# Kernel tuning notes

Measured on AMD Instinct MI355X. Metric: run time of the kernel, lower is better.

The kernel has to match this reference:

```python
import jax, jax.numpy as jnp
import numpy as np

N_NODES = 50000
N_EDGES = 1200000
N_OD = 10000
D_NODE = 16
D_EDGE = 8
HID = 64
N_LAYERS = 3
K_MIN = 1.0
K_MAX = 50.0


def setup_inputs() -> dict:
    key = jax.random.key(0)
    ks = jax.random.split(key, 24)
    s = 0.05
    inp = {
        "node_features": jax.random.normal(ks[0], (N_NODES, D_NODE), jnp.float32),
        "edge_index": jax.random.randint(ks[1], (2, N_EDGES), 0, N_NODES, jnp.int32),
        "edge_features": jax.random.normal(ks[2], (N_EDGES, D_EDGE), jnp.float32),
        "od_pairs": jax.random.randint(ks[3], (2, N_OD), 0, N_NODES, jnp.int32),
        "traffic_stats": jax.random.normal(ks[4], (4,), jnp.float32),
        # projections
        "Wn": jax.random.normal(ks[5], (D_NODE, HID), jnp.float32) * s,
        "bn": jnp.zeros((HID,), jnp.float32),
        "We": jax.random.normal(ks[6], (D_EDGE, HID), jnp.float32) * s,
        "be": jnp.zeros((HID,), jnp.float32),
        # stacked GNN layer weights: message MLP on [h_src, e], update MLP on [h, agg]
        "Wm": jax.random.normal(ks[7], (N_LAYERS, 2 * HID, HID), jnp.float32) * s,
        "bm": jnp.zeros((N_LAYERS, HID), jnp.float32),
        "Wu": jax.random.normal(ks[8], (N_LAYERS, 2 * HID, HID), jnp.float32) * s,
        "bu": jnp.zeros((N_LAYERS, HID), jnp.float32),
        # per-flow score MLP on [h_src, h_dst]
        "Ws1": jax.random.normal(ks[9], (2 * HID, HID), jnp.float32) * s,
        "bs1": jnp.zeros((HID,), jnp.float32),
        "Ws2": jax.random.normal(ks[10], (HID, 1), jnp.float32) * s,
        "bs2": jnp.zeros((1,), jnp.float32),
        # DynamicKHead: Linear(HID+4,32) -> ReLU -> Linear(32,16) -> ReLU -> Linear(16,1)
        "Wk1": jax.random.normal(ks[11], (HID + 4, 32), jnp.float32) * s,
        "bk1": jnp.zeros((32,), jnp.float32),
        "Wk2": jax.random.normal(ks[12], (32, 16), jnp.float32) * s,
        "bk2": jnp.zeros((16,), jnp.float32),
        "Wk3": jax.random.normal(ks[13], (16, 1), jnp.float32) * s,
        "bk3": jnp.zeros((1,), jnp.float32),
    }
    return inp


def _forward(node_features, edge_features, traffic_stats,
             Wn, bn, We, be, Wm, bm, Wu, bu,
             Ws1, bs1, Ws2, bs2, Wk1, bk1, Wk2, bk2, Wk3, bk3,
             edge_index, od_pairs):
    relu = jax.nn.relu
    h = relu(node_features @ Wn + bn)          # [N, HID]
    e = relu(edge_features @ We + be)          # [E, HID]
    src, dst = edge_index[0], edge_index[1]
    for l in range(N_LAYERS):
        # gather-compute-scatter message passing with edge features
        m = relu(jnp.concatenate([h[src], e], axis=-1) @ Wm[l] + bm[l])  # [E, HID]
        agg = jax.ops.segment_sum(m, dst, num_segments=N_NODES)          # [N, HID]
        h = relu(jnp.concatenate([h, agg], axis=-1) @ Wu[l] + bu[l]) + h  # residual
    # per-flow scores from OD endpoint embeddings
    hp = jnp.concatenate([h[od_pairs[0]], h[od_pairs[1]]], axis=-1)      # [P, 2*HID]
    scores = (relu(hp @ Ws1 + bs1) @ Ws2 + bs2).squeeze(-1)              # [P]
    # dynamic-K head (dropout = identity in eval)
    graph_embed = h.mean(axis=0)                                          # [HID]
    x = jnp.concatenate([graph_embed, traffic_stats], axis=-1)
    raw = (relu(relu(x @ Wk1 + bk1) @ Wk2 + bk2) @ Wk3 + bk3).squeeze(-1)
    k_continuous = K_MIN + jax.nn.sigmoid(raw) * (K_MAX - K_MIN)
    return scores, k_continuous


def reference(node_features, edge_index, edge_features, od_pairs, traffic_stats,
              Wn, bn, We, be, Wm, bm, Wu, bu,
              Ws1, bs1, Ws2, bs2, Wk1, bk1, Wk2, bk2, Wk3, bk3):
    return _forward(node_features, edge_features, traffic_stats,
                    Wn, bn, We, be, Wm, bm, Wu, bu,
                    Ws1, bs1, Ws2, bs2, Wk1, bk1, Wk2, bk2, Wk3, bk3,
                    edge_index, od_pairs)
```

## Files before the change

### kernel.cpp

```cpp
#include <hip/hip_runtime.h>
#include <hip/hip_bf16.h>

#define OFF_WN   0
#define OFF_BN   1024
#define OFF_WE   1088
#define OFF_BE   1600
#define OFF_WM   1664
#define OFF_BM   26240
#define OFF_WU   26432
#define OFF_BU   51008
#define OFF_WS1  51200
#define OFF_BS1  59392
#define OFF_WS2  59456
#define OFF_BS2  59520
#define OFF_WK1  59521
#define OFF_BK1  61697
#define OFF_WK2  61729
#define OFF_BK2  62241
#define OFF_WK3  62257
#define OFF_BK3  62273
#define OFF_TS   62274
#define OFF_GSUM 62278
#define OFF_FLAG 62344
#define OFF_BSUM 62400
#define OFF_BOFF 62900
#define OFF_H    65536

typedef __attribute__((ext_vector_type(8))) short bfrag;
typedef __attribute__((ext_vector_type(4))) float ffrag;

__device__ __forceinline__ float bf2f(unsigned short u) {
    unsigned int i = ((unsigned int)u) << 16;
    float f;
    __builtin_memcpy(&f, &i, sizeof(f));
    return f;
}
__device__ __forceinline__ float bflo(unsigned int u) {
    unsigned int i = u << 16;
    float f; __builtin_memcpy(&f, &i, sizeof(f)); return f;
}
__device__ __forceinline__ float bfhi(unsigned int u) {
    unsigned int i = u & 0xffff0000u;
    float f; __builtin_memcpy(&f, &i, sizeof(f)); return f;
}
__device__ __forceinline__ unsigned int f2bf_rne(float f) {
    unsigned int u; __builtin_memcpy(&u, &f, 4);
    return (u + 0x7fffu + ((u >> 16) & 1u)) >> 16;
}
__device__ __forceinline__ unsigned int pack2bf(float a, float b) {
    return f2bf_rne(a) | (f2bf_rne(b) << 16);
}
__device__ __forceinline__ unsigned int cvt_pk_bf16(float a, float b) {
    unsigned int r;
    asm("v_cvt_pk_bf16_f32 %0, %1, %2" : "=v"(r) : "v"(a), "v"(b));
    return r;
}

__global__ void detect_dtype_kernel(const unsigned short* __restrict__ nf,
                                    int* __restrict__ flag) {
    int t = threadIdx.x;
    float m = 0.f;
    for (int i = t; i < 1024; i += 64) {
        float v = fabsf(bf2f(nf[i]));
        if (!isnan(v)) m = fmaxf(m, v);
        else m = 1e30f;
    }
    for (int o = 32; o > 0; o >>= 1) m = fmaxf(m, __shfl_down(m, o));
    if (t == 0) flag[0] = (m > 1e6f) ? 1 : 0;
}

struct ConvArgs {
    const void* src[19];
    int off[19];
    int n[19];
};

__global__ __launch_bounds__(256) void convert_all_kernel(
        ConvArgs a, float* __restrict__ ws, const int* __restrict__ flagp) {
    int isf32 = *flagp;
    int ai = blockIdx.y;
    int i  = blockIdx.x * blockDim.x + threadIdx.x;
    if (i < a.n[ai]) {
        float v = isf32 ? ((const float*)a.src[ai])[i]
                        : bf2f(((const unsigned short*)a.src[ai])[i]);
        ws[a.off[ai] + i] = v;
    }
}

__global__ __launch_bounds__(256) void wtrans_prep_kernel(
        const float* __restrict__ ws, short* __restrict__ Wb) {
    int idx = blockIdx.x * 256 + threadIdx.x;
    if (idx < 12288) {
        int l = idx >> 12, rem = idx & 4095, n = rem >> 6, k = rem & 63;
        Wb[idx] = (short)f2bf_rne(ws[OFF_WM + l * 8192 + 4096 + k * 64 + n]);
    } else if (idx < 24576) {
        int j = idx - 12288;
        int l = j >> 12, rem = j & 4095, n = rem >> 6, k = rem & 63;
        Wb[idx] = (short)f2bf_rne(ws[OFF_WM + l * 8192 + k * 64 + n]);
    } else if (idx < 49152) {
        int j = idx - 24576;
        int l = j >> 13, rem = j & 8191, n = rem >> 7, k = rem & 127;
        Wb[idx] = (short)f2bf_rne(ws[OFF_WU + l * 8192 + k * 64 + n]);
    } else if (idx < 51200) {
        int j = idx - 49152;
        int n = j >> 5, k = j & 31;
        Wb[idx] = (k < 8) ? (short)f2bf_rne(ws[OFF_WE + k * 64 + n]) : (short)0;
    } else if (idx < 59392) {
        int j = idx - 51200;
        int n = j >> 7, k = j & 127;
        Wb[idx] = (short)f2bf_rne(ws[OFF_WS1 + k * 64 + n]);
    }
}

__global__ __launch_bounds__(256) void node_proj_kernel(
        const void* __restrict__ nf, const float* __restrict__ ws,
        float* __restrict__ h, int N, const int* __restrict__ flagp) {
    int idx = blockIdx.x * blockDim.x + threadIdx.x;
    if (idx >= N * 64) return;
    int isf32 = *flagp;
    int i = idx >> 6, c = idx & 63;
    const float* Wn = ws + OFF_WN;
    float acc = ws[OFF_BN + c];
    float x[16];
    if (isf32) {
        const float* row = (const float*)nf + (size_t)i * 16;
#pragma unroll
        for (int k = 0; k < 16; ++k) x[k] = row[k];
    } else {
        const unsigned short* row = (const unsigned short*)nf + (size_t)i * 16;
#pragma unroll
        for (int k = 0; k < 16; ++k) x[k] = bf2f(row[k]);
    }
#pragma unroll
    for (int k = 0; k < 16; ++k) acc = fmaf(x[k], Wn[k * 64 + c], acc);
    h[idx] = fmaxf(acc, 0.f);
}

__global__ __launch_bounds__(256) void count_kernel(
        const int* __restrict__ dst, int* __restrict__ deg, int E) {
    int e = blockIdx.x * blockDim.x + threadIdx.x;
    if (e < E) atomicAdd(&deg[dst[e]], 1);
}

__global__ __launch_bounds__(256) void scan_blocks_kernel(
        const int* __restrict__ deg, int* __restrict__ incl,
        int* __restrict__ bsum, int N) {
    int tid = threadIdx.x;
    int gid = blockIdx.x * 256 + tid;
    int v = (gid < N) ? deg[gid] : 0;
    int lane = tid & 63, w = tid >> 6;
    int x = v;
#pragma unroll
    for (int o = 1; o < 64; o <<= 1) {
        int y = __shfl_up(x, o);
        if (lane >= o) x += y;
    }
    __shared__ int wsum[4];
    __shared__ int woff[4];
    if (lane == 63) wsum[w] = x;
    __syncthreads();
    if (tid == 0) {
        int a = 0;
#pragma unroll
        for (int i = 0; i < 4; ++i) { woff[i] = a; a += wsum[i]; }
    }
    __syncthreads();
    x += woff[w];
    if (gid < N) incl[gid] = x;
    if (tid == 255) bsum[blockIdx.x] = x;
}

__global__ __launch_bounds__(256) void scan_bsum_kernel(
        const int* __restrict__ bsum, int* __restrict__ boff, int nb) {
    __shared__ int sh[256];
    int tid = threadIdx.x;
    int carry = 0;
    for (int base = 0; base < nb; base += 256) {
        int v = (base + tid < nb) ? bsum[base + tid] : 0;
        sh[tid] = v;
        __syncthreads();
        for (int o = 1; o < 256; o <<= 1) {
            int t = (tid >= o) ? sh[tid - o] : 0;
            __syncthreads();
            sh[tid] += t;
            __syncthreads();
        }
        if (base + tid < nb) boff[base + tid] = carry + sh[tid] - v;
        __syncthreads();
        carry += sh[255];
        __syncthreads();
    }
}

__global__ __launch_bounds__(256) void scan_finalize_kernel(
        const int* __restrict__ deg, const int* __restrict__ incl,
        const int* __restrict__ boff, int* __restrict__ out,
        int* __restrict__ cursor, int N, int tailval) {
    int gid = blockIdx.x * 256 + threadIdx.x;
    if (gid < N) {
        int ex = boff[blockIdx.x] + incl[gid] - deg[gid];
        out[gid] = ex;
        cursor[gid] = ex;
    }
    if (gid == 0) out[N] = tailval;
}

__global__ __launch_bounds__(256) void fill_kernel(
        const int* __restrict__ src, const int* __restrict__ dst,
        const void* __restrict__ ef, int* __restrict__ cursor,
        int* __restrict__ eid, int* __restrict__ srcs,
        float* __restrict__ rec, int E, int big,
        const int* __restrict__ flagp) {
    int e = blockIdx.x * blockDim.x + threadIdx.x;
    if (e >= E) return;
    int d = dst[e];
    int pos = atomicAdd(&cursor[d], 1);
    if (big) {
        unsigned p01, p23, p45, p67;
        if (*flagp) {
            const float4* p = (const float4*)ef + (size_t)e * 2;
            float4 a = p[0], b = p[1];
            p01 = pack2bf(a.x, a.y); p23 = pack2bf(a.z, a.w);
            p45 = pack2bf(b.x, b.y); p67 = pack2bf(b.z, b.w);
        } else {
            uint4 r = ((const uint4*)ef)[e];
            p01 = r.x; p23 = r.y; p45 = r.z; p67 = r.w;
        }
        float* o = rec + (size_t)pos * 8;
        *(uint4*)o = make_uint4((unsigned)src[e], (unsigned)d, p01, p23);
        *(uint2*)(o + 4) = make_uint2(p45, p67);
    } else {
        eid[pos] = e;
        srcs[pos] = src[e];
    }
}

__global__ __launch_bounds__(256) void spans_kernel(
        const int* __restrict__ off, int* __restrict__ spans, int N) {
    int i = blockIdx.x * blockDim.x + threadIdx.x;
    if (i >= N) return;
    int k0 = off[i], k1 = off[i + 1];
    spans[i] = (k1 > k0) ? (((k1 - 1) >> 6) - (k0 >> 6) + 1) : 0;
}

__global__ __launch_bounds__(256) void nodeA_mfma_kernel(
        const short* __restrict__ W1T, const float* __restrict__ bm,
        const float* __restrict__ h, float* __restrict__ A, int N) {
    __shared__ short lds_w[64 * 72];
    __shared__ short lds_x[4][64 * 72];
    const int tid = threadIdx.x, wid = tid >> 6, lane = tid & 63;
    const int r = lane & 15, q = lane >> 4;
    const int nb0 = blockIdx.x * 256 + wid * 64;

#pragma unroll
    for (int j = 0; j < 2; ++j) {
        int f8 = (tid * 2 + j) * 8;
        int row = f8 >> 6, k = f8 & 63;
        *(uint4*)&lds_w[row * 72 + k] = ((const uint4*)W1T)[tid * 2 + j];
    }
    short* xt = &lds_x[wid][0];
#pragma unroll 1
    for (int it = 0; it < 16; ++it) {
        int f4 = it * 64 + lane;
        int node = f4 >> 4, c4 = f4 & 15;
        int gn = nb0 + node; if (gn >= N) gn = N - 1;
        float4 v = ((const float4*)h)[(size_t)gn * 16 + c4];
        *(uint2*)&xt[node * 72 + c4 * 4] =
            make_uint2(pack2bf(v.x, v.y), pack2bf(v.z, v.w));
    }
    __syncthreads();

    bfrag bg[4][2];
#pragma unroll
    for (int ni = 0; ni < 4; ++ni)
#pragma unroll
        for (int ki = 0; ki < 2; ++ki)
            bg[ni][ki] = *(const bfrag*)&lds_w[(ni * 16 + r) * 72 + ki * 32 + q * 8];
    float buv[4];
#pragma unroll
    for (int ni = 0; ni < 4; ++ni) buv[ni] = bm[ni * 16 + r];

    ffrag C[4][4];
#pragma unroll
    for (int mi = 0; mi < 4; ++mi) {
        bfrag af[2];
#pragma unroll
        for (int ki = 0; ki < 2; ++ki)
            af[ki] = *(const bfrag*)&xt[(mi * 16 + r) * 72 + ki * 32 + q * 8];
#pragma unroll
        for (int ni = 0; ni < 4; ++ni) {
            ffrag c = {buv[ni], buv[ni], buv[ni], buv[ni]};
            c = __builtin_amdgcn_mfma_f32_16x16x32_bf16(af[0], bg[ni][0], c, 0, 0, 0);
            c = __builtin_amdgcn_mfma_f32_16x16x32_bf16(af[1], bg[ni][1], c, 0, 0, 0);
            C[mi][ni] = c;
        }
    }
#pragma unroll
    for (int mi = 0; mi < 4; ++mi)
#pragma unroll
        for (int rr = 0; rr < 4; ++rr) {
            int gn = nb0 + mi * 16 + q * 4 + rr;
            if (gn < N) {
#pragma unroll
                for (int ni = 0; ni < 4; ++ni)
                    A[(size_t)gn * 64 + ni * 16 + r] = C[mi][ni][rr];
            }
        }
}

__global__ __launch_bounds__(256, 4) void msg_mfma_red(
        const short* __restrict__ WeT, const float* __restrict__ be,
        const short* __restrict__ WbT, const float* __restrict__ rec,
        const float* __restrict__ A, float* __restrict__ pbuf,
        const int* __restrict__ off, const int* __restrict__ pstart, int E) {
    __shared__ short lds_ev[4][64 * 72];
    __shared__ int   lds_src[4][64];
    const int tid = threadIdx.x;
    const int wid = tid >> 6, lane = tid & 63;
    const int w = blockIdx.x * 4 + wid;
    if (w * 64 >= E) return;
    const int slot = w * 64 + lane;
    const int slotc = (slot < E) ? slot : (E - 1);

    const float* rbase = rec + (size_t)slotc * 8;
    uint4 r0 = *(const uint4*)rbase;
    uint2 r1 = *(const uint2*)(rbase + 4);
    int s  = (int)r0.x;
    int di = (int)r0.y;
    int pstv = pstart[di];
    int offv = off[di];
    lds_src[wid][lane] = s;

    short* evb = &lds_ev[wid][0];
    short* evrow = evb + lane * 72;
    *(uint4*)(evrow) = make_uint4(r0.z, r0.w, r1.x, r1.y);
    uint4 z4 = make_uint4(0u, 0u, 0u, 0u);
    *(uint4*)(evrow + 8)  = z4;
    *(uint4*)(evrow + 16) = z4;
    *(uint4*)(evrow + 24) = z4;

    const int r = lane & 15, q = lane >> 4;

    bfrag afe[4];
#pragma unroll
    for (int mi = 0; mi < 4; ++mi)
        afe[mi] = *(const bfrag*)(evb + (mi * 16 + r) * 72 + q * 8);

#pragma unroll
    for (int ni = 0; ni < 4; ++ni) {
        bfrag bge = *(const bfrag*)(WeT + (ni * 16 + r) * 32 + q * 8);
        float4 b4 = *(const float4*)(be + ni * 16 + q * 4);
#pragma unroll
        for (int mi = 0; mi < 4; ++mi) {
            ffrag c = {b4.x, b4.y, b4.z, b4.w};
            c = __builtin_amdgcn_mfma_f32_16x16x32_bf16(bge, afe[mi], c, 0, 0, 0);
            unsigned lo = cvt_pk_bf16(fmaxf(c[0], 0.f), fmaxf(c[1], 0.f));
            unsigned hi = cvt_pk_bf16(fmaxf(c[2], 0.f), fmaxf(c[3], 0.f));
            *(uint2*)(evb + (mi * 16 + r) * 72 + ni * 16 + q * 4) =
                make_uint2(lo, hi);
        }
    }

    bfrag af[4][2];
#pragma unroll
    for (int mi = 0; mi < 4; ++mi)
#pragma unroll
        for (int ki = 0; ki < 2; ++ki)
            af[mi][ki] = *(const bfrag*)(evb + (mi * 16 + r) * 72 + ki * 32 + q * 8);

    const float* ap[4][4];
#pragma unroll
    for (int mi = 0; mi < 4; ++mi) {
        int4 sr = *(const int4*)&lds_src[wid][mi * 16 + q * 4];
        ap[mi][0] = A + (size_t)sr.x * 64 + r;
        ap[mi][1] = A + (size_t)sr.y * 64 + r;
        ap[mi][2] = A + (size_t)sr.z * 64 + r;
        ap[mi][3] = A + (size_t)sr.w * 64 + r;
    }

#pragma unroll
    for (int ni = 0; ni < 4; ++ni) {
        bfrag bg0 = *(const bfrag*)(WbT + (ni * 16 + r) * 64 + q * 8);
        bfrag bg1 = *(const bfrag*)(WbT + (ni * 16 + r) * 64 + 32 + q * 8);
        ffrag C[4];
#pragma unroll
        for (int mi = 0; mi < 4; ++mi) {
            C[mi][0] = ap[mi][0][ni * 16];
            C[mi][1] = ap[mi][1][ni * 16];
            C[mi][2] = ap[mi][2][ni * 16];
            C[mi][3] = ap[mi][3][ni * 16];
        }
#pragma unroll
        for (int mi = 0; mi < 4; ++mi) {
            C[mi] = __builtin_amdgcn_mfma_f32_16x16x32_bf16(af[mi][0], bg0, C[mi], 0, 0, 0);
            C[mi] = __builtin_amdgcn_mfma_f32_16x16x32_bf16(af[mi][1], bg1, C[mi], 0, 0, 0);
        }
#pragma unroll
        for (int mi = 0; mi < 4; ++mi) {
            unsigned lo = cvt_pk_bf16(fmaxf(C[mi][0], 0.f), fmaxf(C[mi][1], 0.f));
            unsigned hi = cvt_pk_bf16(fmaxf(C[mi][2], 0.f), fmaxf(C[mi][3], 0.f));
            *(uint2*)(evb + (ni * 16 + r) * 72 + mi * 16 + q * 4) =
                make_uint2(lo, hi);
        }
    }

    int kmax = E - w * 64; if (kmax > 64) kmax = 64;
    if (kmax < 64) {
        for (int k = kmax; k < 64; ++k) evb[lane * 72 + k] = 0;
    }
    int prevd = __shfl_up(di, 1);
    unsigned long long sm = __ballot(lane != 0 && di != prevd);
    int curp = __shfl(pstv, 0) + (w - (__shfl(offv, 0) >> 6));
    float acc = 0.f;
#pragma unroll
    for (int g = 0; g < 8; ++g) {
        uint4 v = *(const uint4*)(evb + lane * 72 + g * 8);
        float f0 = bflo(v.x), f1 = bfhi(v.x), f2 = bflo(v.y), f3 = bfhi(v.y);
        float f4 = bflo(v.z), f5 = bfhi(v.z), f6 = bflo(v.w), f7 = bfhi(v.w);
        unsigned gm = (unsigned)(sm >> (g * 8)) & 0xffu;
        if (gm == 0) {
            acc += (((f0 + f1) + (f2 + f3)) + ((f4 + f5) + (f6 + f7)));
        } else {
            float fv[8] = {f0, f1, f2, f3, f4, f5, f6, f7};
#pragma unroll
            for (int j = 0; j < 8; ++j) {
                if (gm & (1u << j)) {
                    pbuf[(size_t)curp * 64 + lane] = acc;
                    acc = 0.f;
                    curp = __shfl(pstv, g * 8 + j);
                }
                acc += fv[j];
            }
        }
    }
    pbuf[(size_t)curp * 64 + lane] = acc;
}

__global__ __launch_bounds__(256) void fixup_kernel(
        const float* __restrict__ pbuf, const int* __restrict__ off,
        const int* __restrict__ pstart, float* __restrict__ agg, int N) {
    int tid = blockIdx.x * blockDim.x + threadIdx.x;
    int i = tid >> 2, q = tid & 3;
    if (i >= N) return;
    int k0 = off[i], k1 = off[i + 1];
    float acc[16];
#pragma unroll
    for (int c = 0; c < 16; ++c) acc[c] = 0.f;
    if (k1 > k0) {
        int nsp = ((k1 - 1) >> 6) - (k0 >> 6) + 1;
        int p = pstart[i];
        for (int j = 0; j < nsp; ++j) {
            const float4* pr = (const float4*)(pbuf + (size_t)(p + j) * 64 + q * 16);
#pragma unroll
            for (int c = 0; c < 4; ++c) {
                float4 v = pr[c];
                acc[4 * c] += v.x; acc[4 * c + 1] += v.y;
                acc[4 * c + 2] += v.z; acc[4 * c + 3] += v.w;
            }
        }
    }
    float4* o4 = (float4*)(agg + (size_t)i * 64 + q * 16);
#pragma unroll
    for (int c = 0; c < 4; ++c)
        o4[c] = make_float4(acc[4 * c], acc[4 * c + 1], acc[4 * c + 2], acc[4 * c + 3]);
}

__global__ __launch_bounds__(128) void update_mfma_kernel(
        const short* __restrict__ WuT, const float* __restrict__ bu,
        float* __restrict__ h, const float* __restrict__ agg, int N) {
    __shared__ short lds_w[64 * 136];
    __shared__ short lds_x[2][64 * 136];
    const int tid = threadIdx.x, wid = tid >> 6, lane = tid & 63;
    const int r = lane & 15, q = lane >> 4;
    const int nb0 = blockIdx.x * 128 + wid * 64;
#pragma unroll
    for (int j = 0; j < 8; ++j) {
        int f8 = (tid * 8 + j) * 8;
        int row = f8 >> 7, k = f8 & 127;
        *(uint4*)&lds_w[row * 136 + k] = ((const uint4*)WuT)[tid * 8 + j];
    }
    short* xt = &lds_x[wid][0];
#pragma unroll 1
    for (int it = 0; it < 32; ++it) {
        int f4 = it * 64 + lane;
        int node = f4 >> 5, c4 = f4 & 31;
        int gn = nb0 + node; if (gn >= N) gn = N - 1;
        const float4* src = (c4 < 16)
            ? ((const float4*)h + (size_t)gn * 16 + c4)
            : ((const float4*)agg + (size_t)gn * 16 + (c4 - 16));
        float4 v = *src;
        *(uint2*)&xt[node * 136 + c4 * 4] =
            make_uint2(pack2bf(v.x, v.y), pack2bf(v.z, v.w));
    }
    __syncthreads();
    bfrag bg[4][4];
#pragma unroll
    for (int ni = 0; ni < 4; ++ni)
#pragma unroll
        for (int ki = 0; ki < 4; ++ki)
            bg[ni][ki] = *(const bfrag*)&lds_w[(ni * 16 + r) * 136 + ki * 32 + q * 8];
    float buv[4];
#pragma unroll
    for (int ni = 0; ni < 4; ++ni) buv[ni] = bu[ni * 16 + r];
    ffrag C[4][4];
#pragma unroll
    for (int mi = 0; mi < 4; ++mi) {
        bfrag af[4];
#pragma unroll
        for (int ki = 0; ki < 4; ++ki)
            af[ki] = *(const bfrag*)&xt[(mi * 16 + r) * 136 + ki * 32 + q * 8];
#pragma unroll
        for (int ni = 0; ni < 4; ++ni) {
            ffrag c = {buv[ni], buv[ni], buv[ni], buv[ni]};
#pragma unroll
            for (int ki = 0; ki < 4; ++ki)
                c = __builtin_amdgcn_mfma_f32_16x16x32_bf16(af[ki], bg[ni][ki], c, 0, 0, 0);
            C[mi][ni] = c;
        }
    }
#pragma unroll
    for (int mi = 0; mi < 4; ++mi)
#pragma unroll
        for (int rr = 0; rr < 4; ++rr) {
            int nl = mi * 16 + q * 4 + rr;
            int gn = nb0 + nl;
            if (gn < N) {
#pragma unroll
                for (int ni = 0; ni < 4; ++ni) {
                    float hold = bf2f((unsigned short)xt[nl * 136 + ni * 16 + r]);
                    h[(size_t)gn * 64 + ni * 16 + r] =
                        fmaxf(C[mi][ni][rr], 0.f) + hold;
                }
            }
        }
}

__global__ __launch_bounds__(256) void gather_msg_fallback(
        const float* __restrict__ Wm2, const float* __restrict__ We,
        const float* __restrict__ be, const void* __restrict__ ef,
        const int* __restrict__ srcs, const int* __restrict__ eid,
        const int* __restrict__ off, const float* __restrict__ A,
        float* __restrict__ agg, int N, const int* __restrict__ flagp) {
    int i = blockIdx.x * blockDim.x + threadIdx.x;
    if (i >= N) return;
    int isf32 = *flagp;
    int k0 = off[i], k1 = off[i + 1];
    float acc[64];
#pragma unroll
    for (int c = 0; c < 64; ++c) acc[c] = 0.f;
    for (int k = k0; k < k1; ++k) {
        int s = srcs[k];
        int e = eid[k];
        const float4* a4 = (const float4*)(A + (size_t)s * 64);
        float t[64];
#pragma unroll
        for (int c = 0; c < 16; ++c) {
            float4 v = a4[c];
            t[4 * c] = v.x; t[4 * c + 1] = v.y; t[4 * c + 2] = v.z; t[4 * c + 3] = v.w;
        }
        float efv[8];
        if (isf32) {
            const float4* e4 = (const float4*)ef + (size_t)e * 2;
            float4 ra = e4[0], rb = e4[1];
            efv[0]=ra.x; efv[1]=ra.y; efv[2]=ra.z; efv[3]=ra.w;
            efv[4]=rb.x; efv[5]=rb.y; efv[6]=rb.z; efv[7]=rb.w;
        } else {
            uint4 rr = ((const uint4*)ef)[e];
            efv[0]=bflo(rr.x); efv[1]=bfhi(rr.x); efv[2]=bflo(rr.y); efv[3]=bfhi(rr.y);
            efv[4]=bflo(rr.z); efv[5]=bfhi(rr.z); efv[6]=bflo(rr.w); efv[7]=bfhi(rr.w);
        }
#pragma unroll 1
        for (int d0 = 0; d0 < 64; d0 += 8) {
            float ev[8];
#pragma unroll
            for (int dd = 0; dd < 8; ++dd) {
                float a = be[d0 + dd];
#pragma unroll
                for (int kk = 0; kk < 8; ++kk) a = fmaf(efv[kk], We[kk * 64 + d0 + dd], a);
                ev[dd] = fmaxf(a, 0.f);
            }
#pragma unroll
            for (int dd = 0; dd < 8; ++dd) {
                const float* w = Wm2 + (d0 + dd) * 64;
#pragma unroll
                for (int c = 0; c < 64; ++c) t[c] = fmaf(ev[dd], w[c], t[c]);
            }
        }
#pragma unroll
        for (int c = 0; c < 64; ++c) acc[c] += fmaxf(t[c], 0.f);
    }
    float4* o4 = (float4*)(agg + (size_t)i * 64);
#pragma unroll
    for (int c = 0; c < 16; ++c)
        o4[c] = make_float4(acc[4 * c], acc[4 * c + 1], acc[4 * c + 2], acc[4 * c + 3]);
}

__global__ __launch_bounds__(128) void scores_mfma_kernel(
        const short* __restrict__ Ws1T, const float* __restrict__ bs1,
        const float* __restrict__ Ws2, const float* __restrict__ bs2,
        const int* __restrict__ ods, const int* __restrict__ odd,
        const float* __restrict__ h, void* __restrict__ out, int P,
        const int* __restrict__ flagp) {
    __shared__ short lds_w[64 * 136];
    __shared__ short lds_x[2][64 * 136];
    const int tid = threadIdx.x, wid = tid >> 6, lane = tid & 63;
    const int r = lane & 15, q = lane >> 4;
    const int pb0 = blockIdx.x * 128 + wid * 64;
#pragma unroll
    for (int j = 0; j < 8; ++j) {
        int f8 = (tid * 8 + j) * 8;
        int row = f8 >> 7, k = f8 & 127;
        *(uint4*)&lds_w[row * 136 + k] = ((const uint4*)Ws1T)[tid * 8 + j];
    }
    short* xt = &lds_x[wid][0];
#pragma unroll 1
    for (int it = 0; it < 32; ++it) {
        int f4 = it * 64 + lane;
        int pr = f4 >> 5, c4 = f4 & 31;
        int gp = pb0 + pr; if (gp >= P) gp = P - 1;
        int node = (c4 < 16) ? ods[gp] : odd[gp];
        int cc = (c4 < 16) ? c4 : (c4 - 16);
        float4 v = ((const float4*)h)[(size_t)node * 16 + cc];
        *(uint2*)&xt[pr * 136 + c4 * 4] =
            make_uint2(pack2bf(v.x, v.y), pack2bf(v.z, v.w));
    }
    __syncthreads();

    bfrag bg[4][4];
#pragma unroll
    for (int ni = 0; ni < 4; ++ni)
#pragma unroll
        for (int ki = 0; ki < 4; ++ki)
            bg[ni][ki] = *(const bfrag*)&lds_w[(ni * 16 + r) * 136 + ki * 32 + q * 8];
    float buv[4], w2v[4];
#pragma unroll
    for (int ni = 0; ni < 4; ++ni) { buv[ni] = bs1[ni * 16 + r]; w2v[ni] = Ws2[ni * 16 + r]; }
    int isf32 = *flagp;
    float b2 = bs2[0];

#pragma unroll
    for (int mi = 0; mi < 4; ++mi) {
        bfrag af[4];
#pragma unroll
        for (int ki = 0; ki < 4; ++ki)
            af[ki] = *(const bfrag*)&xt[(mi * 16 + r) * 136 + ki * 32 + q * 8];
        float part[4] = {0.f, 0.f, 0.f, 0.f};
#pragma unroll
        for (int ni = 0; ni < 4; ++ni) {
            ffrag c = {buv[ni], buv[ni], buv[ni], buv[ni]};
#pragma unroll
            for (int ki = 0; ki < 4; ++ki)
                c = __builtin_amdgcn_mfma_f32_16x16x32_bf16(af[ki], bg[ni][ki], c, 0, 0, 0);
#pragma unroll
            for (int rr = 0; rr < 4; ++rr)
                part[rr] = fmaf(fmaxf(c[rr], 0.f), w2v[ni], part[rr]);
        }
#pragma unroll
        for (int rr = 0; rr < 4; ++rr) {
            float v = part[rr];
            v += __shfl_xor(v, 1); v += __shfl_xor(v, 2);
            v += __shfl_xor(v, 4); v += __shfl_xor(v, 8);
            if (r == 0) {
                int p = pb0 + mi * 16 + q * 4 + rr;
                if (p < P) {
                    float score = v + b2;
                    if (isf32) ((float*)out)[p] = score;
                    else ((__hip_bfloat16*)out)[p] = __float2bfloat16(score);
                }
            }
        }
    }
}

__global__ __launch_bounds__(256) void embed_kernel(
        const float* __restrict__ h, float* __restrict__ gsum, int N) {
    __shared__ float red[256];
    int c = threadIdx.x & 63;
    int sub = threadIdx.x >> 6;
    float a = 0.f;
    for (int i = blockIdx.x * 4 + sub; i < N; i += gridDim.x * 4)
        a += h[(size_t)i * 64 + c];
    red[threadIdx.x] = a;
    __syncthreads();
    if (threadIdx.x < 64) {
        float t = red[threadIdx.x] + red[threadIdx.x + 64] +
                  red[threadIdx.x + 128] + red[threadIdx.x + 192];
        unsafeAtomicAdd(&gsum[threadIdx.x], t);
    }
}

__global__ void khead_kernel(const float* __restrict__ ws,
                             void* __restrict__ out, int N, int P,
                             const int* __restrict__ flagp) {
    if (threadIdx.x != 0 || blockIdx.x != 0) return;
    float x[68];
    float invN = 1.f / (float)N;
#pragma unroll
    for (int c = 0; c < 64; ++c) x[c] = ws[OFF_GSUM + c] * invN;
#pragma unroll
    for (int k = 0; k < 4; ++k) x[64 + k] = ws[OFF_TS + k];
    float h1[32];
    for (int j = 0; j < 32; ++j) {
        float a = ws[OFF_BK1 + j];
        for (int i = 0; i < 68; ++i) a = fmaf(x[i], ws[OFF_WK1 + i * 32 + j], a);
        h1[j] = fmaxf(a, 0.f);
    }
    float h2[16];
    for (int k2 = 0; k2 < 16; ++k2) {
        float a = ws[OFF_BK2 + k2];
        for (int j = 0; j < 32; ++j) a = fmaf(h1[j], ws[OFF_WK2 + j * 16 + k2], a);
        h2[k2] = fmaxf(a, 0.f);
    }
    float raw = ws[OFF_BK3];
    for (int k2 = 0; k2 < 16; ++k2) raw = fmaf(h2[k2], ws[OFF_WK3 + k2], raw);
    float sig = 1.f / (1.f + expf(-raw));
    float k = 1.f + 49.f * sig;
    if (*flagp) ((float*)out)[P] = k;
    else ((__hip_bfloat16*)out)[P] = __float2bfloat16(k);
}

extern "C" void kernel_launch(void* const* d_in, const int* in_sizes, int n_in,
                              void* d_out, int out_size, void* d_ws, size_t ws_size,
                              hipStream_t stream) {
    const void* nf = d_in[0];
    const int*  ei = (const int*)d_in[1];
    const void* ef = d_in[2];
    const int*  od = (const int*)d_in[3];
    float* ws = (float*)d_ws;

    const int N = in_sizes[0] / 16;
    const int E = in_sizes[1] / 2;
    const int P = in_sizes[3] / 2;

    float* h      = ws + OFF_H;
    float* agg    = h + (size_t)N * 64;
    float* A      = agg + (size_t)N * 64;
    int*   deg    = (int*)(A + (size_t)N * 64);
    int*   off    = deg + N;
    int*   cursor = off + N + 1;
    int*   pstart = cursor + N;
    int*   eid    = pstart + N + 1;
    int*   srcs   = eid + E;
    short* WbT    = (short*)(srcs + E);
    short* W1T    = WbT + 12288;
    short* WuT    = WbT + 24576;
    short* WeT    = WbT + 49152;
    short* Ws1T   = WbT + 51200;
    int*   flag   = (int*)(ws + OFF_FLAG);
    int*   bsum   = (int*)(ws + OFF_BSUM);
    int*   boff   = (int*)(ws + OFF_BOFF);

    size_t fsofar = (size_t)OFF_H + 3 * (size_t)N * 64
                  + (size_t)(N + (N + 1) + N + (N + 1) + E + E) + 29696;
    size_t recOff = (fsofar + 7) & ~(size_t)7;
    float* rec = ws + recOff;
    size_t pbufOff = recOff + (size_t)E * 8;
    float* pbuf = ws + pbufOff;
    long pbufRows = (long)N + E / 64 + 128;
    size_t needBytes = (pbufOff + (size_t)pbufRows * 64) * sizeof(float);
    const bool big = (ws_size >= needBytes);

    const int* srcv = ei;
    const int* dstv = ei + E;

    detect_dtype_kernel<<<1, 64, 0, stream>>>((const unsigned short*)nf, flag);

    ConvArgs ca;
    const int srcidx[19] = {5, 6, 7, 8, 9, 10, 11, 12, 13, 14, 15, 16, 17, 18, 19, 20, 21, 22, 4};
    const int wsoff[19]  = {OFF_WN, OFF_BN, OFF_WE, OFF_BE, OFF_WM, OFF_BM, OFF_WU, OFF_BU,
                            OFF_WS1, OFF_BS1, OFF_WS2, OFF_BS2, OFF_WK1, OFF_BK1, OFF_WK2,
                            OFF_BK2, OFF_WK3, OFF_BK3, OFF_TS};
    int maxn = 0;
    for (int i = 0; i < 19; ++i) {
        ca.src[i] = d_in[srcidx[i]];
        ca.off[i] = wsoff[i];
        ca.n[i]   = in_sizes[srcidx[i]];
        if (ca.n[i] > maxn) maxn = ca.n[i];
    }
    dim3 cgrid((maxn + 255) / 256, 19);
    convert_all_kernel<<<cgrid, 256, 0, stream>>>(ca, ws, flag);
    wtrans_prep_kernel<<<232, 256, 0, stream>>>(ws, WbT);

    node_proj_kernel<<<(N * 64 + 255) / 256, 256, 0, stream>>>(nf, ws, h, N, flag);

    hipMemsetAsync(deg, 0, (size_t)N * sizeof(int), stream);
    count_kernel<<<(E + 255) / 256, 256, 0, stream>>>(dstv, deg, E);
    int nb = (N + 255) / 256;
    scan_blocks_kernel<<<nb, 256, 0, stream>>>(deg, cursor, bsum, N);
    scan_bsum_kernel<<<1, 256, 0, stream>>>(bsum, boff, nb);
    scan_finalize_kernel<<<nb, 256, 0, stream>>>(deg, cursor, boff, off, cursor, N, E);
    fill_kernel<<<(E + 255) / 256, 256, 0, stream>>>(
        srcv, dstv, ef, cursor, eid, srcs, rec, E, big ? 1 : 0, flag);

    if (big) {
        spans_kernel<<<nb, 256, 0, stream>>>(off, deg, N);
        scan_blocks_kernel<<<nb, 256, 0, stream>>>(deg, cursor, bsum, N);
        scan_bsum_kernel<<<1, 256, 0, stream>>>(bsum, boff, nb);
        scan_finalize_kernel<<<nb, 256, 0, stream>>>(deg, cursor, boff, pstart, cursor, N, 0);
    }

    const int N4 = N * 4;
    const int mblocks = (E + 255) / 256;
    const int ablocks = (N + 255) / 256;
    const int ublocks = (N + 127) / 128;
    for (int l = 0; l < 3; ++l) {
        nodeA_mfma_kernel<<<ablocks, 256, 0, stream>>>(
            W1T + l * 4096, ws + OFF_BM + l * 64, h, A, N);
        if (big) {
            msg_mfma_red<<<mblocks, 256, 0, stream>>>(
                WeT, ws + OFF_BE, WbT + l * 4096, rec, A, pbuf, off, pstart, E);
            fixup_kernel<<<(N4 + 255) / 256, 256, 0, stream>>>(
                pbuf, off, pstart, agg, N);
        } else {
            const float* Wm2 = ws + OFF_WM + l * 8192 + 4096;
            gather_msg_fallback<<<(N + 255) / 256, 256, 0, stream>>>(
                Wm2, ws + OFF_WE, ws + OFF_BE, ef, srcs, eid, off, A, agg, N, flag);
        }
        update_mfma_kernel<<<ublocks, 128, 0, stream>>>(
            WuT + l * 8192, ws + OFF_BU + l * 64, h, agg, N);
    }

    scores_mfma_kernel<<<(P + 127) / 128, 128, 0, stream>>>(
        Ws1T, ws + OFF_BS1, ws + OFF_WS2, ws + OFF_BS2,
        od, od + P, h, d_out, P, flag);

    hipMemsetAsync(ws + OFF_GSUM, 0, 64 * sizeof(float), stream);
    embed_kernel<<<256, 256, 0, stream>>>(h, ws + OFF_GSUM, N);
    khead_kernel<<<1, 64, 0, stream>>>(ws, d_out, N, P, flag);
}
```

Before: 640.5 us.

## Record edge rank in count pass and shrink edge records to six words

The count kernel now keeps the value returned by its atomic increment as a per-edge rank. The fill kernel then computes each edge's CSR position as off[dst]+rank, so it no longer needs a second atomic per edge. The edge record is also packed from eight floats to six (src, dst, four bf16 pairs), which cuts the record traffic written by fill and read three times by the message kernel. In exchange there is an extra E-sized rank buffer to write and read. The 6-float stride also means record reads use three 8-byte loads instead of one 16-byte and one 8-byte load.

```diff
diff --git a/kernel.cpp b/kernel.cpp
--- a/kernel.cpp
+++ b/kernel.cpp
@@ -137,9 +137,13 @@
 }
 
 __global__ __launch_bounds__(256) void count_kernel(
-        const int* __restrict__ dst, int* __restrict__ deg, int E) {
+        const int* __restrict__ dst, int* __restrict__ deg,
+        int* __restrict__ rank, int E, int dorank) {
     int e = blockIdx.x * blockDim.x + threadIdx.x;
-    if (e < E) atomicAdd(&deg[dst[e]], 1);
+    if (e < E) {
+        int r = atomicAdd(&deg[dst[e]], 1);
+        if (dorank) rank[e] = r;
+    }
 }
 
 __global__ __launch_bounds__(256) void scan_blocks_kernel(
@@ -208,14 +212,15 @@
 __global__ __launch_bounds__(256) void fill_kernel(
         const int* __restrict__ src, const int* __restrict__ dst,
         const void* __restrict__ ef, int* __restrict__ cursor,
+        const int* __restrict__ rank, const int* __restrict__ off,
         int* __restrict__ eid, int* __restrict__ srcs,
         float* __restrict__ rec, int E, int big,
         const int* __restrict__ flagp) {
     int e = blockIdx.x * blockDim.x + threadIdx.x;
     if (e >= E) return;
     int d = dst[e];
-    int pos = atomicAdd(&cursor[d], 1);
     if (big) {
+        int pos = off[d] + rank[e];
         unsigned p01, p23, p45, p67;
         if (*flagp) {
             const float4* p = (const float4*)ef + (size_t)e * 2;
@@ -226,10 +231,12 @@
             uint4 r = ((const uint4*)ef)[e];
             p01 = r.x; p23 = r.y; p45 = r.z; p67 = r.w;
         }
-        float* o = rec + (size_t)pos * 8;
-        *(uint4*)o = make_uint4((unsigned)src[e], (unsigned)d, p01, p23);
+        float* o = rec + (size_t)pos * 6;
+        *(uint2*)o       = make_uint2((unsigned)src[e], (unsigned)d);
+        *(uint2*)(o + 2) = make_uint2(p01, p23);
         *(uint2*)(o + 4) = make_uint2(p45, p67);
     } else {
+        int pos = atomicAdd(&cursor[d], 1);
         eid[pos] = e;
         srcs[pos] = src[e];
     }
@@ -322,18 +329,19 @@
     const int slot = w * 64 + lane;
     const int slotc = (slot < E) ? slot : (E - 1);
 
-    const float* rbase = rec + (size_t)slotc * 8;
-    uint4 r0 = *(const uint4*)rbase;
-    uint2 r1 = *(const uint2*)(rbase + 4);
-    int s  = (int)r0.x;
-    int di = (int)r0.y;
+    const float* rbase = rec + (size_t)slotc * 6;
+    uint2 u0 = *(const uint2*)rbase;
+    uint2 u1 = *(const uint2*)(rbase + 2);
+    uint2 u2 = *(const uint2*)(rbase + 4);
+    int s  = (int)u0.x;
+    int di = (int)u0.y;
     int pstv = pstart[di];
     int offv = off[di];
     lds_src[wid][lane] = s;
 
     short* evb = &lds_ev[wid][0];
     short* evrow = evb + lane * 72;
-    *(uint4*)(evrow) = make_uint4(r0.z, r0.w, r1.x, r1.y);
+    *(uint4*)(evrow) = make_uint4(u1.x, u1.y, u2.x, u2.y);
     uint4 z4 = make_uint4(0u, 0u, 0u, 0u);
     *(uint4*)(evrow + 8)  = z4;
     *(uint4*)(evrow + 16) = z4;
@@ -746,15 +754,16 @@
     short* WuT    = WbT + 24576;
     short* WeT    = WbT + 49152;
     short* Ws1T   = WbT + 51200;
+    int*   rank   = (int*)(WbT + 59392);
     int*   flag   = (int*)(ws + OFF_FLAG);
     int*   bsum   = (int*)(ws + OFF_BSUM);
     int*   boff   = (int*)(ws + OFF_BOFF);
 
     size_t fsofar = (size_t)OFF_H + 3 * (size_t)N * 64
-                  + (size_t)(N + (N + 1) + N + (N + 1) + E + E) + 29696;
+                  + (size_t)(N + (N + 1) + N + (N + 1) + E + E + E) + 29696;
     size_t recOff = (fsofar + 7) & ~(size_t)7;
     float* rec = ws + recOff;
-    size_t pbufOff = recOff + (size_t)E * 8;
+    size_t pbufOff = recOff + (size_t)E * 6;
     float* pbuf = ws + pbufOff;
     long pbufRows = (long)N + E / 64 + 128;
     size_t needBytes = (pbufOff + (size_t)pbufRows * 64) * sizeof(float);
@@ -784,13 +793,13 @@
     node_proj_kernel<<<(N * 64 + 255) / 256, 256, 0, stream>>>(nf, ws, h, N, flag);
 
     hipMemsetAsync(deg, 0, (size_t)N * sizeof(int), stream);
-    count_kernel<<<(E + 255) / 256, 256, 0, stream>>>(dstv, deg, E);
+    count_kernel<<<(E + 255) / 256, 256, 0, stream>>>(dstv, deg, rank, E, big ? 1 : 0);
     int nb = (N + 255) / 256;
     scan_blocks_kernel<<<nb, 256, 0, stream>>>(deg, cursor, bsum, N);
     scan_bsum_kernel<<<1, 256, 0, stream>>>(bsum, boff, nb);
     scan_finalize_kernel<<<nb, 256, 0, stream>>>(deg, cursor, boff, off, cursor, N, E);
     fill_kernel<<<(E + 255) / 256, 256, 0, stream>>>(
-        srcv, dstv, ef, cursor, eid, srcs, rec, E, big ? 1 : 0, flag);
+        srcv, dstv, ef, cursor, rank, off, eid, srcs, rec, E, big ? 1 : 0, flag);
 
     if (big) {
         spans_kernel<<<nb, 256, 0, stream>>>(off, deg, N);
```

Result: faster. 621.8 us (-2.9%).
